# Kernel tuning notes

Hardware: AMD Instinct MI355X
Metric: run time of the kernel (lower is better)

The kernel has to match this reference:

```python
import jax, jax.numpy as jnp
import numpy as np

B, S, D = 2, 2048, 4096
NH, NKV, HD = 32, 8, 128
NREP = NH // NKV
ROPE_THETA = 10000.0


def setup_inputs() -> dict:
    key = jax.random.key(0)
    k1, k2, k3, k4, k5 = jax.random.split(key, 5)
    x = jax.random.normal(k1, (B, S, D), jnp.float32)
    wq = jax.random.normal(k2, (NH * HD, D), jnp.float32) * 0.02
    wk = jax.random.normal(k3, (NKV * HD, D), jnp.float32) * 0.02
    wv = jax.random.normal(k4, (NKV * HD, D), jnp.float32) * 0.02
    wo = jax.random.normal(k5, (D, NH * HD), jnp.float32) * 0.02
    inv_freq = 1.0 / (ROPE_THETA ** (np.arange(0, HD, 2, dtype=np.float64) / HD))
    ang = np.outer(np.arange(S, dtype=np.float64), inv_freq)  # [S, HD/2]
    return {
        'x': x, 'start_pos': 0,
        'freqs_cos': jnp.asarray(np.cos(ang), jnp.float32),
        'freqs_sin': jnp.asarray(np.sin(ang), jnp.float32),
        'wq': wq, 'wk': wk, 'wv': wv, 'wo': wo,
    }


def _apply_rope(x, cos, sin):
    # x: [B, S, H, HD]; cos/sin: [S, HD/2]. Matches torch view_as_complex on
    # interleaved (even, odd) feature pairs: (xr + i*xi) * (cos + i*sin).
    xr = x[..., 0::2]
    xi = x[..., 1::2]
    c = cos[None, :, None, :]
    s = sin[None, :, None, :]
    out_r = xr * c - xi * s
    out_i = xr * s + xi * c
    return jnp.stack([out_r, out_i], axis=-1).reshape(x.shape)


def reference(x, start_pos, freqs_cos, freqs_sin, wq, wk, wv, wo):
    b, s, _ = x.shape
    xq = (x @ wq.T).reshape(b, s, NH, HD)
    xk = (x @ wk.T).reshape(b, s, NKV, HD)
    xv = (x @ wv.T).reshape(b, s, NKV, HD)
    # Source applies RoPE to K and V (not Q) -- reproduced faithfully.
    xk = _apply_rope(xk, freqs_cos, freqs_sin)
    xv = _apply_rope(xv, freqs_cos, freqs_sin)
    # start_pos == 0 prefill: cache slice [:, :start_pos+s] == freshly written xk/xv.
    # repeat_kv: head h_out = h_kv * NREP + rep  ==  jnp.repeat along head axis.
    keys = jnp.repeat(xk, NREP, axis=2)    # [B, S, NH, HD]
    values = jnp.repeat(xv, NREP, axis=2)  # [B, S, NH, HD]
    scale = 1.0 / jnp.sqrt(jnp.asarray(HD, x.dtype))
    scores = jnp.einsum('bqhd,bkhd->bhqk', xq, keys) * scale  # [B, NH, S, S]
    probs = jax.nn.softmax(scores, axis=-1)  # NOTE: no causal mask in source
    out = jnp.einsum('bhqk,bkhd->bqhd', probs, values).reshape(b, s, NH * HD)
    return out @ wo.T
```

## Files before the change

### kernel.cpp

```cpp
#include <hip/hip_runtime.h>


typedef short bf16x8 __attribute__((ext_vector_type(8)));
typedef float f32x4 __attribute__((ext_vector_type(4)));

__device__ __forceinline__ void load16(const void* g, void* l) {
  __builtin_amdgcn_global_load_lds(
      (const __attribute__((address_space(1))) void*)g,
      (__attribute__((address_space(3))) void*)l, 16, 0, 0);
}

__device__ __forceinline__ f32x4 mfma16(bf16x8 a, bf16x8 b, f32x4 c) {
  return __builtin_amdgcn_mfma_f32_16x16x32_bf16(a, b, c, 0, 0, 0);
}

__device__ __forceinline__ unsigned short f2b(float f) {
  union { float f; unsigned int u; } v; v.f = f;
  unsigned int u = v.u;
  return (unsigned short)((u + 0x7fffu + ((u >> 16) & 1u)) >> 16);
}
__device__ __forceinline__ float b2f(unsigned short u) {
  union { unsigned int u; float f; } v; v.u = ((unsigned int)u) << 16;
  return v.f;
}

#define QSCALE (0.08838834764831845f * 1.4426950408889634f)

__global__ __launch_bounds__(256) void cvt_f32_bf16(
    const float* __restrict__ in, unsigned short* __restrict__ out, int n4) {
  int idx = blockIdx.x * 256 + threadIdx.x;
  int stride = gridDim.x * 256;
  for (int i = idx; i < n4; i += stride) {
    float4 v = reinterpret_cast<const float4*>(in)[i];
    ushort4 o;
    o.x = f2b(v.x); o.y = f2b(v.y); o.z = f2b(v.z); o.w = f2b(v.w);
    reinterpret_cast<ushort4*>(out)[i] = o;
  }
}

template <typename OutT, bool SCALEQ>
__global__ __launch_bounds__(512, 2) void gemm256(
    const unsigned short* __restrict__ A, const unsigned short* __restrict__ Bw,
    OutT* __restrict__ C, int M, int N, int K) {
  extern __shared__ char smem[];
  const int tid = threadIdx.x;
  const int lane = tid & 63;
  const int w = tid >> 6;
  const int lr = lane & 15, lg = lane >> 4;
  const int wr = w >> 2, wc = w & 3;

  const int nbn = N >> 8;
  const int bid = blockIdx.x, nwg = gridDim.x;
  const int swz = (bid & 7) * (nwg >> 3) + (bid >> 3);
  const int bm = swz / nbn, bn = swz % nbn;

  const unsigned short* Ab = A + (size_t)bm * 256 * K;
  const unsigned short* Bb = Bw + (size_t)bn * 256 * K;

  int mS[2], kS[2];
#pragma unroll
  for (int r = 0; r < 2; ++r) {
    int L = r * 8192 + tid * 16;
    int U = L ^ (((L >> 9) & 1) << 5);
    mS[r] = U >> 6;
    kS[r] = (U & 63) >> 1;
  }
  const int wavebase = (tid & ~63) * 16;

  f32x4 acc[8][4];
#pragma unroll
  for (int m = 0; m < 8; ++m)
#pragma unroll
    for (int n = 0; n < 4; ++n) acc[m][n] = (f32x4){0.f, 0.f, 0.f, 0.f};

#define STAGE_A(tt)                                                          \
  {                                                                          \
    char* dst = smem + ((tt)&3) * 32768;                                     \
    _Pragma("unroll") for (int r = 0; r < 2; ++r)                            \
        load16(Ab + (size_t)mS[r] * K + (tt)*32 + kS[r],                     \
               dst + r * 8192 + wavebase);                                   \
  }
#define STAGE_B(tt)                                                          \
  {                                                                          \
    char* dst = smem + ((tt)&3) * 32768 + 16384;                             \
    _Pragma("unroll") for (int r = 0; r < 2; ++r)                            \
        load16(Bb + (size_t)mS[r] * K + (tt)*32 + kS[r],                     \
               dst + r * 8192 + wavebase);                                   \
  }

  for (int tt = 0; tt < 3; ++tt) { STAGE_A(tt); STAGE_B(tt); }

  const int NT = K >> 5;
  const int xorb = ((lr >> 3) & 1) << 5;
  const int aRowBase = (wr * 128 + lr) * 64 + lg * 16;
  const int bRowBase = (wc * 64 + lr) * 64 + lg * 16;

  for (int t = 0; t < NT; ++t) {
    const int rem = NT - 1 - t;
    if (rem >= 2)      asm volatile("s_waitcnt vmcnt(8)" ::: "memory");
    else if (rem == 1) asm volatile("s_waitcnt vmcnt(4)" ::: "memory");
    else               asm volatile("s_waitcnt vmcnt(0)" ::: "memory");
    __builtin_amdgcn_s_barrier();

    const char* buf = smem + (t & 3) * 32768;
    bf16x8 a0[4], b0[4];
#pragma unroll
    for (int mf = 0; mf < 4; ++mf)
      a0[mf] = *(const bf16x8*)(buf + ((aRowBase + mf * 16 * 64) ^ xorb));
#pragma unroll
    for (int nf = 0; nf < 4; ++nf)
      b0[nf] = *(const bf16x8*)(buf + 16384 + ((bRowBase + nf * 16 * 64) ^ xorb));
    if (t + 3 < NT) STAGE_A(t + 3);
    __builtin_amdgcn_s_barrier();
    asm volatile("s_waitcnt lgkmcnt(0)" ::: "memory");
    __builtin_amdgcn_sched_barrier(0);
    __builtin_amdgcn_s_setprio(1);
#pragma unroll
    for (int mf = 0; mf < 4; ++mf)
#pragma unroll
      for (int nf = 0; nf < 4; ++nf)
        acc[mf][nf] = mfma16(a0[mf], b0[nf], acc[mf][nf]);
    __builtin_amdgcn_s_setprio(0);
    __builtin_amdgcn_s_barrier();
    bf16x8 a1[4];
#pragma unroll
    for (int mf = 0; mf < 4; ++mf)
      a1[mf] = *(const bf16x8*)(buf + ((aRowBase + (4 + mf) * 16 * 64) ^ xorb));
    if (t + 3 < NT) STAGE_B(t + 3);
    __builtin_amdgcn_s_barrier();
    asm volatile("s_waitcnt lgkmcnt(0)" ::: "memory");
    __builtin_amdgcn_sched_barrier(0);
    __builtin_amdgcn_s_setprio(1);
#pragma unroll
    for (int mf = 0; mf < 4; ++mf)
#pragma unroll
      for (int nf = 0; nf < 4; ++nf)
        acc[4 + mf][nf] = mfma16(a1[mf], b0[nf], acc[4 + mf][nf]);
    __builtin_amdgcn_s_setprio(0);
  }
#undef STAGE_A
#undef STAGE_B

#pragma unroll
  for (int mf = 0; mf < 8; ++mf)
#pragma unroll
    for (int nf = 0; nf < 4; ++nf)
#pragma unroll
      for (int r = 0; r < 4; ++r) {
        int rowc = bm * 256 + wr * 128 + mf * 16 + lg * 4 + r;
        int colc = bn * 256 + wc * 64 + nf * 16 + lr;
        float v = acc[mf][nf][r];
        if constexpr (SCALEQ) v *= QSCALE;
        if constexpr (sizeof(OutT) == 2)
          C[(size_t)rowc * N + colc] = (OutT)f2b(v);
        else
          C[(size_t)rowc * N + colc] = v;
      }
}

template <typename OutT>
__global__ __launch_bounds__(256) void gemm_bt(
    const unsigned short* __restrict__ A, const unsigned short* __restrict__ Bw,
    OutT* __restrict__ C, int M, int N, int K) {
  alignas(16) __shared__ unsigned short As[4][128][8];
  alignas(16) __shared__ unsigned short Bs[4][128][8];
  const int t = threadIdx.x;
  const int lane = t & 63, w = t >> 6;
  const int lr = lane & 15, lg = lane >> 4;
  const int wr = w >> 1, wc = w & 1;

  const int nbn = N >> 7;
  const int nwg = gridDim.x;
  const int bid = blockIdx.x;
  const int swz = (bid & 7) * (nwg >> 3) + (bid >> 3);
  const int bm = swz / nbn, bn = swz % nbn;

  f32x4 acc[4][4];
#pragma unroll
  for (int m = 0; m < 4; ++m)
#pragma unroll
    for (int n = 0; n < 4; ++n) acc[m][n] = (f32x4){0.f, 0.f, 0.f, 0.f};

  const int c0 = t, c1 = 256 + t;
  const int kc0 = c0 >> 7, row0 = c0 & 127;
  const int kc1 = c1 >> 7, row1 = c1 & 127;
  const unsigned short* Ab = A + (size_t)(bm * 128) * K;
  const unsigned short* Bb = Bw + (size_t)(bn * 128) * K;
  char* AsB = (char*)&As[0][0][0];
  char* BsB = (char*)&Bs[0][0][0];
  const int ub0 = (t & 192) * 16;
  const int ub1 = (256 + (t & 192)) * 16;

  for (int k0 = 0; k0 < K; k0 += 32) {
    load16(Ab + (size_t)row0 * K + k0 + kc0 * 8, AsB + ub0);
    load16(Ab + (size_t)row1 * K + k0 + kc1 * 8, AsB + ub1);
    load16(Bb + (size_t)row0 * K + k0 + kc0 * 8, BsB + ub0);
    load16(Bb + (size_t)row1 * K + k0 + kc1 * 8, BsB + ub1);
    __syncthreads();
    bf16x8 af[4], bfr[4];
#pragma unroll
    for (int i = 0; i < 4; ++i)
      af[i] = *(const bf16x8*)&As[lg][wr * 64 + i * 16 + lr][0];
#pragma unroll
    for (int i = 0; i < 4; ++i)
      bfr[i] = *(const bf16x8*)&Bs[lg][wc * 64 + i * 16 + lr][0];
#pragma unroll
    for (int m = 0; m < 4; ++m)
#pragma unroll
      for (int n = 0; n < 4; ++n)
        acc[m][n] = mfma16(af[m], bfr[n], acc[m][n]);
    __syncthreads();
  }

#pragma unroll
  for (int m = 0; m < 4; ++m)
#pragma unroll
    for (int n = 0; n < 4; ++n)
#pragma unroll
      for (int r = 0; r < 4; ++r) {
        int rowc = bm * 128 + wr * 64 + m * 16 + lg * 4 + r;
        int colc = bn * 128 + wc * 64 + n * 16 + lr;
        float v = acc[m][n][r];
        if constexpr (sizeof(OutT) == 2)
          C[(size_t)rowc * N + colc] = (OutT)f2b(v);
        else
          C[(size_t)rowc * N + colc] = v;
      }
}

__global__ __launch_bounds__(256) void rope_kv(
    const unsigned short* __restrict__ XKV,
    const float* __restrict__ fc, const float* __restrict__ fs,
    unsigned short* __restrict__ Kr, unsigned short* __restrict__ Vt) {
  __shared__ unsigned short Vl[128][66];
  const int t = threadIdx.x;
  const int bid = blockIdx.x;
  const int stile = bid & 31, bkv = bid >> 5;
  const int b = bkv >> 3, kvh = bkv & 7;
  const int s0 = stile * 64;
  const int l = t & 63;
  const int jrow = t >> 6;

  for (int j = 0; j < 16; ++j) {
    int s = s0 + j * 4 + jrow;
    ushort2 v = *(const ushort2*)(XKV + (size_t)(b * 2048 + s) * 2048 + kvh * 128 + 2 * l);
    float c = fc[s * 64 + l], sn = fs[s * 64 + l];
    float xr = b2f(v.x), xi = b2f(v.y);
    ushort2 o;
    o.x = f2b(xr * c - xi * sn);
    o.y = f2b(xr * sn + xi * c);
    *(ushort2*)(Kr + ((size_t)bkv * 2048 + s) * 128 + 2 * l) = o;
  }
  for (int j = 0; j < 16; ++j) {
    int ss = j * 4 + jrow;
    int s = s0 + ss;
    ushort2 v = *(const ushort2*)(XKV + (size_t)(b * 2048 + s) * 2048 + 1024 + kvh * 128 + 2 * l);
    float c = fc[s * 64 + l], sn = fs[s * 64 + l];
    float xr = b2f(v.x), xi = b2f(v.y);
    Vl[2 * l][ss] = f2b(xr * c - xi * sn);
    Vl[2 * l + 1][ss] = f2b(xr * sn + xi * c);
  }
  __syncthreads();
  const int d = t >> 1, half = t & 1;
  unsigned short* vdst = Vt + ((size_t)bkv * 128 + d) * 2048 + s0 + half * 32;
#pragma unroll
  for (int e = 0; e < 32; e += 4) {
    ushort4 pk;
    pk.x = Vl[d][half * 32 + e];
    pk.y = Vl[d][half * 32 + e + 1];
    pk.z = Vl[d][half * 32 + e + 2];
    pk.w = Vl[d][half * 32 + e + 3];
    *(ushort4*)(vdst + e) = pk;
  }
}

__global__ __launch_bounds__(256, 3) void attn_fwd(
    const unsigned short* __restrict__ XQ, const unsigned short* __restrict__ Kr,
    const unsigned short* __restrict__ Vt, unsigned short* __restrict__ AO) {
  alignas(16) __shared__ char Ksm[2][8192];
  alignas(16) __shared__ char Vsm[2][8192];
  alignas(16) __shared__ unsigned short Ps[4][32][72];
  const int t = threadIdx.x;
  const int lane = t & 63, w = t >> 6;
  const int lr = lane & 15, lg = lane >> 4;

  const int bid = blockIdx.x;
  const int nwg = gridDim.x;
  const int swz = (bid & 7) * (nwg >> 3) + (bid >> 3);
  const int qt = swz & 15;
  const int bh = swz >> 4;
  const int b = bh >> 5, h = bh & 31;
  const int bkv = b * 8 + (h >> 2);

  bf16x8 qf[2][4];
#pragma unroll
  for (int q2 = 0; q2 < 2; ++q2) {
    const unsigned short* qp =
        XQ + ((size_t)(b * 2048 + qt * 128 + w * 32 + q2 * 16 + lr)) * 4096 +
        h * 128 + lg * 8;
#pragma unroll
    for (int dc = 0; dc < 4; ++dc) qf[q2][dc] = *(const bf16x8*)(qp + dc * 32);
  }

  f32x4 acc[2][8];
#pragma unroll
  for (int q2 = 0; q2 < 2; ++q2)
#pragma unroll
    for (int i = 0; i < 8; ++i) acc[q2][i] = (f32x4){0.f, 0.f, 0.f, 0.f};
  float l_[2][4] = {{0.f, 0.f, 0.f, 0.f}, {0.f, 0.f, 0.f, 0.f}};

  const unsigned short* Kbase = Kr + (size_t)bkv * 2048 * 128;
  const unsigned short* Vbase = Vt + (size_t)bkv * 128 * 2048;

  const int c0 = t, c1 = t + 256;
  const int kRow0 = c0 >> 4, kOff0 = ((c0 & 15) ^ ((c0 >> 4) & 7)) << 3;
  const int kRow1 = c1 >> 4, kOff1 = ((c1 & 15) ^ ((c1 >> 4) & 7)) << 3;
  const int vRow0 = c0 >> 2, vOff0 = ((c0 & 3) ^ ((c0 >> 3) & 3)) << 3;
  const int vRow1 = c1 >> 2, vOff1 = ((c1 & 3) ^ ((c1 >> 3) & 3)) << 3;
  const int dstb0 = (c0 & ~63) * 16;
  const int dstb1 = (c1 & ~63) * 16;

#define STAGE_KV(bufi, kt)                                                    \
  {                                                                           \
    load16(Kbase + (size_t)((kt)*32 + kRow0) * 128 + kOff0, Ksm[bufi] + dstb0); \
    load16(Kbase + (size_t)((kt)*32 + kRow1) * 128 + kOff1, Ksm[bufi] + dstb1); \
    load16(Vbase + (size_t)vRow0 * 2048 + (kt)*32 + vOff0, Vsm[bufi] + dstb0);  \
    load16(Vbase + (size_t)vRow1 * 2048 + (kt)*32 + vOff1, Vsm[bufi] + dstb1);  \
  }

  STAGE_KV(0, 0);
  asm volatile("s_waitcnt vmcnt(0)" ::: "memory");
  __builtin_amdgcn_s_barrier();

  const int kfx = (lr & 7) << 4;
  const int vfx = ((lr >> 1) & 3) << 4;

  for (int kt = 0; kt < 64; ++kt) {
    const int cur = kt & 1;
    if (kt < 63) STAGE_KV(cur ^ 1, kt + 1);

    const char* Kc = Ksm[cur];
    const char* Vc = Vsm[cur];

#pragma unroll
    for (int nf = 0; nf < 2; ++nf) {
      f32x4 s0 = (f32x4){0.f, 0.f, 0.f, 0.f};
      f32x4 s1 = (f32x4){0.f, 0.f, 0.f, 0.f};
#pragma unroll
      for (int dc = 0; dc < 4; ++dc) {
        bf16x8 kf = *(const bf16x8*)(Kc + (nf * 16 + lr) * 256 +
                                     ((dc * 64 + lg * 16) ^ kfx));
        s0 = mfma16(qf[0][dc], kf, s0);
        s1 = mfma16(qf[1][dc], kf, s1);
      }
#pragma unroll
      for (int r = 0; r < 4; ++r) {
        float p0 = __builtin_amdgcn_exp2f(s0[r]);
        float p1 = __builtin_amdgcn_exp2f(s1[r]);
        l_[0][r] += p0;
        l_[1][r] += p1;
        Ps[w][lg * 4 + r][nf * 16 + lr] = f2b(p0);
        Ps[w][16 + lg * 4 + r][nf * 16 + lr] = f2b(p1);
      }
    }

    bf16x8 pf0 = *(const bf16x8*)((const char*)&Ps[w][lr][0] + lg * 16);
    bf16x8 pf1 = *(const bf16x8*)((const char*)&Ps[w][16 + lr][0] + lg * 16);
#pragma unroll
    for (int dt = 0; dt < 8; ++dt) {
      bf16x8 vf = *(const bf16x8*)(Vc + (dt * 16 + lr) * 64 + ((lg * 16) ^ vfx));
      acc[0][dt] = mfma16(pf0, vf, acc[0][dt]);
      acc[1][dt] = mfma16(pf1, vf, acc[1][dt]);
    }

    asm volatile("s_waitcnt vmcnt(0)" ::: "memory");
    __builtin_amdgcn_s_barrier();
  }
#undef STAGE_KV

#pragma unroll
  for (int q2 = 0; q2 < 2; ++q2)
#pragma unroll
    for (int r = 0; r < 4; ++r) {
#pragma unroll
      for (int o = 1; o < 16; o <<= 1) l_[q2][r] += __shfl_xor(l_[q2][r], o);
    }

#pragma unroll
  for (int q2 = 0; q2 < 2; ++q2)
#pragma unroll
    for (int r = 0; r < 4; ++r) {
      float inv = 1.f / l_[q2][r];
      size_t rowb =
          ((size_t)(b * 2048 + qt * 128 + w * 32 + q2 * 16 + lg * 4 + r)) * 4096 +
          h * 128;
#pragma unroll
      for (int dt = 0; dt < 8; ++dt)
        AO[rowb + dt * 16 + lr] = f2b(acc[q2][dt][r] * inv);
    }
}

extern "C" void kernel_launch(void* const* d_in, const int* in_sizes, int n_in,
                              void* d_out, int out_size, void* d_ws, size_t ws_size,
                              hipStream_t stream) {
  const float* x  = (const float*)d_in[0];
  const float* fc = (const float*)d_in[2];
  const float* fs = (const float*)d_in[3];
  const float* wq = (const float*)d_in[4];
  const float* wk = (const float*)d_in[5];
  const float* wv = (const float*)d_in[6];
  const float* wo = (const float*)d_in[7];

  const size_t MB = 1024ull * 1024ull;
  char* ws = (char*)d_ws;
  unsigned short* Xb  = (unsigned short*)(ws);
  unsigned short* Wsc = (unsigned short*)(ws + 32 * MB);
  unsigned short* XKV = (unsigned short*)(ws + 64 * MB);
  unsigned short* Kr  = (unsigned short*)(ws);
  unsigned short* Vt  = (unsigned short*)(ws + 8 * MB);
  unsigned short* AO  = (unsigned short*)(ws + 80 * MB);
  unsigned short* XQ  = (unsigned short*)d_out;

  (void)hipFuncSetAttribute((const void*)gemm256<unsigned short, true>,
                            hipFuncAttributeMaxDynamicSharedMemorySize, 131072);
  (void)hipFuncSetAttribute((const void*)gemm256<float, false>,
                            hipFuncAttributeMaxDynamicSharedMemorySize, 131072);

  dim3 blk(256);
  dim3 blk512(512);
  cvt_f32_bf16<<<2048, blk, 0, stream>>>(x, Xb, (2 * 2048 * 4096) / 4);
  cvt_f32_bf16<<<2048, blk, 0, stream>>>(wq, Wsc, (4096 * 4096) / 4);
  gemm256<unsigned short, true><<<256, blk512, 131072, stream>>>(
      Xb, Wsc, XQ, 4096, 4096, 4096);
  cvt_f32_bf16<<<2048, blk, 0, stream>>>(wk, Wsc, (1024 * 4096) / 4);
  cvt_f32_bf16<<<2048, blk, 0, stream>>>(wv, Wsc + 1024 * 4096, (1024 * 4096) / 4);
  gemm_bt<unsigned short><<<512, blk, 0, stream>>>(Xb, Wsc, XKV, 4096, 2048, 4096);
  rope_kv<<<512, blk, 0, stream>>>(XKV, fc, fs, Kr, Vt);
  attn_fwd<<<1024, blk, 0, stream>>>(XQ, Kr, Vt, AO);
  cvt_f32_bf16<<<2048, blk, 0, stream>>>(wo, Wsc, (4096 * 4096) / 4);
  gemm256<float, false><<<256, blk512, 131072, stream>>>(
      AO, Wsc, (float*)d_out, 4096, 4096, 4096);
}
```

Before: 626.5 us.

## Use chunk-major LDS layouts for K, V and P tiles; raise occupancy and add setprio

Replaces the XOR-swizzled K and V shared-memory tiles with a chunk-major layout, where consecutive lanes read consecutive 16-byte chunks. The P scratch is repacked the same way, which also shrinks its padded footprint. These layouts are meant to give conflict-free ds_read_b128 fragment loads without the swizzle arithmetic. The change also raises launch_bounds occupancy from 3 to 4 waves per SIMD and wraps the MFMA loops in s_setprio to favour matrix issue. The denser global gather pattern for staging, and register pressure at the higher occupancy target, may cost something.

```diff
diff --git a/kernel.cpp b/kernel.cpp
--- a/kernel.cpp
+++ b/kernel.cpp
@@ -274,12 +274,12 @@
   }
 }
 
-__global__ __launch_bounds__(256, 3) void attn_fwd(
+__global__ __launch_bounds__(256, 4) void attn_fwd(
     const unsigned short* __restrict__ XQ, const unsigned short* __restrict__ Kr,
     const unsigned short* __restrict__ Vt, unsigned short* __restrict__ AO) {
   alignas(16) __shared__ char Ksm[2][8192];
   alignas(16) __shared__ char Vsm[2][8192];
-  alignas(16) __shared__ unsigned short Ps[4][32][72];
+  alignas(16) __shared__ unsigned short Ps[4][4][32][8];
   const int t = threadIdx.x;
   const int lane = t & 63, w = t >> 6;
   const int lr = lane & 15, lg = lane >> 4;
@@ -313,27 +313,27 @@
   const unsigned short* Vbase = Vt + (size_t)bkv * 128 * 2048;
 
   const int c0 = t, c1 = t + 256;
-  const int kRow0 = c0 >> 4, kOff0 = ((c0 & 15) ^ ((c0 >> 4) & 7)) << 3;
-  const int kRow1 = c1 >> 4, kOff1 = ((c1 & 15) ^ ((c1 >> 4) & 7)) << 3;
-  const int vRow0 = c0 >> 2, vOff0 = ((c0 & 3) ^ ((c0 >> 3) & 3)) << 3;
-  const int vRow1 = c1 >> 2, vOff1 = ((c1 & 3) ^ ((c1 >> 3) & 3)) << 3;
+  const int kK0 = c0 & 31, dC0 = c0 >> 5;
+  const int kK1 = c1 & 31, dC1 = c1 >> 5;
+  const int vD0 = c0 & 127, vKc0 = c0 >> 7;
+  const int vD1 = c1 & 127, vKc1 = c1 >> 7;
   const int dstb0 = (c0 & ~63) * 16;
   const int dstb1 = (c1 & ~63) * 16;
 
-#define STAGE_KV(bufi, kt)                                                    \
-  {                                                                           \
-    load16(Kbase + (size_t)((kt)*32 + kRow0) * 128 + kOff0, Ksm[bufi] + dstb0); \
-    load16(Kbase + (size_t)((kt)*32 + kRow1) * 128 + kOff1, Ksm[bufi] + dstb1); \
-    load16(Vbase + (size_t)vRow0 * 2048 + (kt)*32 + vOff0, Vsm[bufi] + dstb0);  \
-    load16(Vbase + (size_t)vRow1 * 2048 + (kt)*32 + vOff1, Vsm[bufi] + dstb1);  \
+#define STAGE_KV(bufi, kt)                                                     \
+  {                                                                            \
+    load16(Kbase + (size_t)((kt)*32 + kK0) * 128 + dC0 * 8, Ksm[bufi] + dstb0);\
+    load16(Kbase + (size_t)((kt)*32 + kK1) * 128 + dC1 * 8, Ksm[bufi] + dstb1);\
+    load16(Vbase + (size_t)vD0 * 2048 + (kt)*32 + vKc0 * 8, Vsm[bufi] + dstb0);\
+    load16(Vbase + (size_t)vD1 * 2048 + (kt)*32 + vKc1 * 8, Vsm[bufi] + dstb1);\
   }
 
   STAGE_KV(0, 0);
   asm volatile("s_waitcnt vmcnt(0)" ::: "memory");
   __builtin_amdgcn_s_barrier();
 
-  const int kfx = (lr & 7) << 4;
-  const int vfx = ((lr >> 1) & 3) << 4;
+  unsigned short* Pw = &Ps[w][0][0][0];
+  const int pbase = (lr >> 3) * 256 + (lr & 7);
 
   for (int kt = 0; kt < 64; ++kt) {
     const int cur = kt & 1;
@@ -346,32 +346,37 @@
     for (int nf = 0; nf < 2; ++nf) {
       f32x4 s0 = (f32x4){0.f, 0.f, 0.f, 0.f};
       f32x4 s1 = (f32x4){0.f, 0.f, 0.f, 0.f};
+      __builtin_amdgcn_s_setprio(1);
 #pragma unroll
       for (int dc = 0; dc < 4; ++dc) {
-        bf16x8 kf = *(const bf16x8*)(Kc + (nf * 16 + lr) * 256 +
-                                     ((dc * 64 + lg * 16) ^ kfx));
+        bf16x8 kf =
+            *(const bf16x8*)(Kc + ((dc * 4 + lg) * 32 + nf * 16 + lr) * 16);
         s0 = mfma16(qf[0][dc], kf, s0);
         s1 = mfma16(qf[1][dc], kf, s1);
       }
+      __builtin_amdgcn_s_setprio(0);
+      const int pb = pbase + nf * 512;
 #pragma unroll
       for (int r = 0; r < 4; ++r) {
         float p0 = __builtin_amdgcn_exp2f(s0[r]);
         float p1 = __builtin_amdgcn_exp2f(s1[r]);
         l_[0][r] += p0;
         l_[1][r] += p1;
-        Ps[w][lg * 4 + r][nf * 16 + lr] = f2b(p0);
-        Ps[w][16 + lg * 4 + r][nf * 16 + lr] = f2b(p1);
+        Pw[pb + (lg * 4 + r) * 8] = f2b(p0);
+        Pw[pb + (16 + lg * 4 + r) * 8] = f2b(p1);
       }
     }
 
-    bf16x8 pf0 = *(const bf16x8*)((const char*)&Ps[w][lr][0] + lg * 16);
-    bf16x8 pf1 = *(const bf16x8*)((const char*)&Ps[w][16 + lr][0] + lg * 16);
+    bf16x8 pf0 = *(const bf16x8*)(Pw + (lg * 32 + lr) * 8);
+    bf16x8 pf1 = *(const bf16x8*)(Pw + (lg * 32 + 16 + lr) * 8);
+    __builtin_amdgcn_s_setprio(1);
 #pragma unroll
     for (int dt = 0; dt < 8; ++dt) {
-      bf16x8 vf = *(const bf16x8*)(Vc + (dt * 16 + lr) * 64 + ((lg * 16) ^ vfx));
+      bf16x8 vf = *(const bf16x8*)(Vc + (lg * 128 + dt * 16 + lr) * 16);
       acc[0][dt] = mfma16(pf0, vf, acc[0][dt]);
       acc[1][dt] = mfma16(pf1, vf, acc[1][dt]);
     }
+    __builtin_amdgcn_s_setprio(0);
 
     asm volatile("s_waitcnt vmcnt(0)" ::: "memory");
     __builtin_amdgcn_s_barrier();
```

After: 667.7 us. +6.6%, slower.
